# Kernel optimization log

Hardware: AMD Instinct MI355X
Metric: run time of the kernel (lower is better)

The kernel has to match this reference:

```python
import jax, jax.numpy as jnp
import numpy as np

N = 170000      # nodes (ogbn-arxiv scale)
E = 2720000     # edges (avg degree 16)
IN, H, L, OUT = 128, 256, 4, 40
BN_EPS = 1e-5


def setup_inputs() -> dict:
    key = jax.random.key(0)
    ks = jax.random.split(key, 6)
    x = jax.random.normal(ks[0], (N, IN), jnp.float32)
    edge_index = jax.random.randint(ks[1], (2, E), 0, N, dtype=jnp.int64)
    W_in = jax.random.normal(ks[2], (IN, H), jnp.float32) * 0.05
    b_in = jnp.zeros((H,), jnp.float32)
    W_hid = jax.random.normal(ks[3], (L - 1, H, H), jnp.float32) * 0.05
    b_hid = jnp.zeros((L - 1, H), jnp.float32)
    gamma = jnp.ones((L, H), jnp.float32)
    beta = jnp.zeros((L, H), jnp.float32)
    W_out = jax.random.normal(ks[4], (L * H, OUT), jnp.float32) * 0.05
    b_out = jnp.zeros((OUT,), jnp.float32)
    return dict(x=x, edge_index=edge_index, W_in=W_in, b_in=b_in,
                W_hid=W_hid, b_hid=b_hid, gamma=gamma, beta=beta,
                W_out=W_out, b_out=b_out)


def _gcn_aggregate(h, src, dst, norm_e, inv_deg):
    # message passing with symmetric normalization + self-loop term
    msg = h[src] * norm_e[:, None]                      # [E, H] gather
    agg = jax.ops.segment_sum(msg, dst, num_segments=N)  # [N, H] scatter-add
    return agg + h * inv_deg[:, None]                   # self-loop: deg^-1


def reference(x, edge_index, W_in, b_in, W_hid, b_hid, gamma, beta, W_out, b_out):
    src, dst = edge_index[0], edge_index[1]
    # degree (incl. self-loop), PyG gcn_norm style
    deg = jax.ops.segment_sum(jnp.ones((E,), x.dtype), dst, num_segments=N) + 1.0
    dinv = jax.lax.rsqrt(deg)
    norm_e = dinv[src] * dinv[dst]
    inv_deg = 1.0 / deg

    outs = []
    h = x
    for i in range(L):
        W = W_in if i == 0 else W_hid[i - 1]
        b = b_in if i == 0 else b_hid[i - 1]
        h = _gcn_aggregate(h @ W, src, dst, norm_e, inv_deg) + b
        # BatchNorm1d (training-mode batch statistics, biased variance)
        mean = jnp.mean(h, axis=0)
        var = jnp.mean(jnp.square(h - mean), axis=0)
        h = (h - mean) * jax.lax.rsqrt(var + BN_EPS) * gamma[i] + beta[i]
        h = jax.nn.relu(h)  # dropout is identity in eval mode
        outs.append(h)

    z = jnp.concatenate(outs, axis=-1) @ W_out + b_out  # JK 'cat' -> [N, L*H] @ [L*H, OUT]
    return jax.nn.log_softmax(z, axis=-1)
```

## Files before the change

kernel.cpp:

```cpp
#include <hip/hip_runtime.h>
#include <math.h>

constexpr int kN = 170000;
constexpr int kE = 2720000;
constexpr int kFin = 128;
constexpr int kFh = 256;
constexpr int kL = 4;
constexpr int kFout = 40;

typedef __attribute__((ext_vector_type(8))) short bf16x8;
typedef __attribute__((ext_vector_type(4))) float f32x4;

__device__ __forceinline__ float jk_b2f(unsigned short u) {
    unsigned int x = ((unsigned int)u) << 16;
    float f;
    __builtin_memcpy(&f, &x, 4);
    return f;
}
__device__ __forceinline__ unsigned short jk_f2b(float f) {
    unsigned int x;
    __builtin_memcpy(&x, &f, 4);
    unsigned int r = (x + 0x7fffu + ((x >> 16) & 1u)) >> 16;
    return (unsigned short)r;
}

union U4 {
    uint4 v;
    unsigned short s[8];
};

__global__ void jk5_zero_i(int* p, int n) {
    int i = blockIdx.x * blockDim.x + threadIdx.x;
    if (i < n) p[i] = 0;
}
__global__ void jk5_zero_f(float* p, int n) {
    int i = blockIdx.x * blockDim.x + threadIdx.x;
    if (i < n) p[i] = 0.0f;
}

__global__ void jk5_detect(const int* eb, int* flag) {
    __shared__ int nz;
    if (threadIdx.x == 0) nz = 0;
    __syncthreads();
    int bad = 0;
    for (int j = 0; j < 4; j++) {
        int idx = threadIdx.x * 4 + j;
        if (eb[2 * idx + 1] != 0) bad = 1;
    }
    if (bad) atomicOr(&nz, 1);
    __syncthreads();
    if (threadIdx.x == 0) {
        flag[0] = nz ? 0 : 1;
        flag[1] = 0;
    }
}

__global__ void jk5_count(const int* eb, const int* flag, int* counts, int* rank) {
    int e = blockIdx.x * blockDim.x + threadIdx.x;
    if (e >= kE) return;
    int s64 = flag[0];
    int d = eb[(kE + e) << s64];
    rank[e] = atomicAdd(&counts[d], 1);
}

__global__ void jk5_nodeprep(const int* counts, float* dinv, float* invdeg, int* off,
                             int* cursor) {
    int n = blockIdx.x * blockDim.x + threadIdx.x;
    if (n < kN) {
        int c = counts[n];
        float deg = (float)c + 1.0f;
        dinv[n] = rsqrtf(deg);
        invdeg[n] = 1.0f / deg;
        off[n] = atomicAdd(cursor, c);
    }
}

__global__ void jk5_fill(const int* eb, const int* flag, const int* rank, const int* off,
                         const float* dinv, int* csr_src, float* csr_w) {
    int e = blockIdx.x * blockDim.x + threadIdx.x;
    if (e >= kE) return;
    int s64 = flag[0];
    int s = eb[e << s64];
    int d = eb[(kE + e) << s64];
    int p = off[d] + rank[e];
    csr_src[p] = s;
    csr_w[p] = dinv[s] * dinv[d];
}

__global__ void jk5_wt(const float* W, unsigned short* Wt, int K) {
    int idx = blockIdx.x * blockDim.x + threadIdx.x;
    if (idx >= K * kFh) return;
    int c = idx / K, k = idx % K;
    Wt[idx] = jk_f2b(W[(size_t)k * kFh + c]);
}

__global__ void jk5_wtout(const float* Wout, unsigned short* Wto) {
    int idx = blockIdx.x * blockDim.x + threadIdx.x;
    if (idx >= kL * 48 * 256) return;
    int l = idx / (48 * 256);
    int rem = idx % (48 * 256);
    int col = rem >> 8, k = rem & 255;
    float wv = (col < kFout) ? Wout[(size_t)(l * kFh + k) * kFout + col] : 0.f;
    unsigned short hi = jk_f2b(wv);
    float res = wv - jk_b2f(hi);
    unsigned short lo = jk_f2b(res);
    Wto[((size_t)(l * 2 + 0) * 48 + col) * 256 + k] = hi;
    Wto[((size_t)(l * 2 + 1) * 48 + col) * 256 + k] = lo;
}

template <int AF32>
__global__ __launch_bounds__(256) void jk5_gemm(const void* Aptr, const unsigned short* Wt,
                                                unsigned short* C, int K) {
    __shared__ unsigned short As[128][40];
    __shared__ unsigned short Bs[128][40];
    int tid = threadIdx.x;
    int row0 = blockIdx.x * 128;
    int n0 = blockIdx.y * 128;
    int lane = tid & 63, w = tid >> 6;
    int wm = w >> 1, wn = w & 1;
    int lr = lane & 15, lg = lane >> 4;

    f32x4 acc[4][4];
#pragma unroll
    for (int i = 0; i < 4; i++)
#pragma unroll
        for (int j = 0; j < 4; j++) acc[i][j] = (f32x4){0.f, 0.f, 0.f, 0.f};

    int sr = tid >> 1;
    int skh = (tid & 1) * 16;

    for (int k0 = 0; k0 < K; k0 += 32) {
        {
            int row = row0 + sr;
            if (AF32) {
                const float* A = (const float*)Aptr;
                unsigned short tmp[16];
                if (row < kN) {
                    const float* g = A + (size_t)row * K + k0 + skh;
#pragma unroll
                    for (int j = 0; j < 16; j++) tmp[j] = jk_f2b(g[j]);
                } else {
#pragma unroll
                    for (int j = 0; j < 16; j++) tmp[j] = 0;
                }
                *(uint4*)&As[sr][skh] = *(uint4*)&tmp[0];
                *(uint4*)&As[sr][skh + 8] = *(uint4*)&tmp[8];
            } else {
                const unsigned short* A = (const unsigned short*)Aptr;
                uint4 u0 = make_uint4(0, 0, 0, 0), u1 = make_uint4(0, 0, 0, 0);
                if (row < kN) {
                    const unsigned short* g = A + (size_t)row * K + k0 + skh;
                    u0 = *(const uint4*)g;
                    u1 = *(const uint4*)(g + 8);
                }
                *(uint4*)&As[sr][skh] = u0;
                *(uint4*)&As[sr][skh + 8] = u1;
            }
        }
        {
            const unsigned short* g = Wt + (size_t)(n0 + sr) * K + k0 + skh;
            *(uint4*)&Bs[sr][skh] = *(const uint4*)g;
            *(uint4*)&Bs[sr][skh + 8] = *(const uint4*)(g + 8);
        }
        __syncthreads();

        bf16x8 af[4], bfr[4];
#pragma unroll
        for (int mi = 0; mi < 4; mi++)
            af[mi] = *(const bf16x8*)&As[wm * 64 + mi * 16 + lr][lg * 8];
#pragma unroll
        for (int ni = 0; ni < 4; ni++)
            bfr[ni] = *(const bf16x8*)&Bs[wn * 64 + ni * 16 + lr][lg * 8];
#pragma unroll
        for (int mi = 0; mi < 4; mi++)
#pragma unroll
            for (int ni = 0; ni < 4; ni++)
                acc[mi][ni] = __builtin_amdgcn_mfma_f32_16x16x32_bf16(af[mi], bfr[ni],
                                                                      acc[mi][ni], 0, 0, 0);
        __syncthreads();
    }

#pragma unroll
    for (int mi = 0; mi < 4; mi++) {
#pragma unroll
        for (int j = 0; j < 4; j++) {
            int row = row0 + wm * 64 + mi * 16 + lg * 4 + j;
            if (row < kN) {
#pragma unroll
                for (int ni = 0; ni < 4; ni++) {
                    int col = n0 + wn * 64 + ni * 16 + lr;
                    C[(size_t)row * kFh + col] = jk_f2b(acc[mi][ni][j]);
                }
            }
        }
    }
}

__global__ __launch_bounds__(256) void jk5_agg(const unsigned short* t, const float* bias,
                                               const int* off, const int* cnt, const int* csr_src,
                                               const float* csr_w, const float* invdeg,
                                               unsigned short* h, float* stats) {
    __shared__ float lsum[256], lsq[256];
    int tid = threadIdx.x;
    lsum[tid] = 0.f;
    lsq[tid] = 0.f;
    int lane32 = tid & 31;
    int grp = tid >> 5;
    int c0 = lane32 * 8;
    float bs[8];
#pragma unroll
    for (int j = 0; j < 8; j++) bs[j] = bias[c0 + j];

    float rsum[8] = {}, rsq[8] = {};

    for (int n = blockIdx.x * 8 + grp; n < kN; n += gridDim.x * 8) {
        float acc[8];
        {
            U4 u;
            u.v = *(const uint4*)(t + (size_t)n * kFh + c0);
            float sw = invdeg[n];
#pragma unroll
            for (int j = 0; j < 8; j++) acc[j] = sw * jk_b2f(u.s[j]);
        }
        int base = off[n], c = cnt[n];
        for (int i = 0; i < c; i += 4) {
            float w[4];
            U4 uu[4];
#pragma unroll
            for (int q = 0; q < 4; q++) {
                int e = i + q;
                bool v = e < c;
                int idx = v ? base + e : base;
                int src = csr_src[idx];
                w[q] = v ? csr_w[idx] : 0.0f;
                uu[q].v = *(const uint4*)(t + (size_t)src * kFh + c0);
            }
#pragma unroll
            for (int q = 0; q < 4; q++)
#pragma unroll
                for (int j = 0; j < 8; j++) acc[j] += w[q] * jk_b2f(uu[q].s[j]);
        }
        U4 o;
#pragma unroll
        for (int j = 0; j < 8; j++) {
            float v = acc[j] + bs[j];
            rsum[j] += v;
            rsq[j] += v * v;
            o.s[j] = jk_f2b(v);
        }
        *(uint4*)(h + (size_t)n * kFh + c0) = o.v;
    }

    __syncthreads();
#pragma unroll
    for (int j = 0; j < 8; j++) {
        atomicAdd(&lsum[c0 + j], rsum[j]);
        atomicAdd(&lsq[c0 + j], rsq[j]);
    }
    __syncthreads();
    atomicAdd(&stats[tid], lsum[tid]);
    atomicAdd(&stats[256 + tid], lsq[tid]);
}

__global__ void jk5_bnfinal(const float* stats, const float* gamma, const float* beta, int layer,
                            float* scale, float* shift) {
    int c = threadIdx.x;
    float mean = stats[c] / (float)kN;
    float var = stats[256 + c] / (float)kN - mean * mean;
    var = var < 0.f ? 0.f : var;
    float sc = gamma[layer * kFh + c] * rsqrtf(var + 1e-5f);
    scale[c] = sc;
    shift[c] = beta[layer * kFh + c] - mean * sc;
}

template <int FIRST, int LAST>
__global__ __launch_bounds__(256) void jk5_zacc(unsigned short* h, const float* scale,
                                                const float* shift, const unsigned short* Wto,
                                                const float* bout, float* z, float* out) {
    __shared__ unsigned short Bs[2][48][264];
    __shared__ unsigned short As[128][40];
    __shared__ float ssc[256], ssh[256];
    int tid = threadIdx.x;
    for (int f = tid; f < 2 * 48 * 256; f += 256) {
        int hl = f / (48 * 256);
        int rem = f % (48 * 256);
        Bs[hl][rem >> 8][rem & 255] = Wto[f];
    }
    ssc[tid] = scale[tid];
    ssh[tid] = shift[tid];
    __syncthreads();

    int row0 = blockIdx.x * 128;
    int w = tid >> 6, lane = tid & 63;
    int lr = lane & 15, lg = lane >> 4;
    int sr = tid >> 1, skh = (tid & 1) * 16;

    f32x4 acc[2][3];
#pragma unroll
    for (int mi = 0; mi < 2; mi++)
#pragma unroll
        for (int ni = 0; ni < 3; ni++) acc[mi][ni] = (f32x4){0.f, 0.f, 0.f, 0.f};

    for (int k0 = 0; k0 < kFh; k0 += 32) {
        int row = row0 + sr;
        U4 o0, o1;
        if (row < kN) {
            U4 u0, u1;
            const unsigned short* g = h + (size_t)row * kFh + k0 + skh;
            u0.v = *(const uint4*)g;
            u1.v = *(const uint4*)(g + 8);
#pragma unroll
            for (int j = 0; j < 8; j++) {
                float v = jk_b2f(u0.s[j]) * ssc[k0 + skh + j] + ssh[k0 + skh + j];
                o0.s[j] = jk_f2b(v > 0.f ? v : 0.f);
            }
#pragma unroll
            for (int j = 0; j < 8; j++) {
                float v = jk_b2f(u1.s[j]) * ssc[k0 + skh + 8 + j] + ssh[k0 + skh + 8 + j];
                o1.s[j] = jk_f2b(v > 0.f ? v : 0.f);
            }
            if (!LAST) {
                *(uint4*)(h + (size_t)row * kFh + k0 + skh) = o0.v;
                *(uint4*)(h + (size_t)row * kFh + k0 + skh + 8) = o1.v;
            }
        } else {
#pragma unroll
            for (int j = 0; j < 8; j++) { o0.s[j] = 0; o1.s[j] = 0; }
        }
        *(uint4*)&As[sr][skh] = o0.v;
        *(uint4*)&As[sr][skh + 8] = o1.v;
        __syncthreads();

        bf16x8 af[2], bh[3], bl[3];
#pragma unroll
        for (int mi = 0; mi < 2; mi++)
            af[mi] = *(const bf16x8*)&As[w * 32 + mi * 16 + lr][lg * 8];
#pragma unroll
        for (int ni = 0; ni < 3; ni++) {
            bh[ni] = *(const bf16x8*)&Bs[0][ni * 16 + lr][k0 + lg * 8];
            bl[ni] = *(const bf16x8*)&Bs[1][ni * 16 + lr][k0 + lg * 8];
        }
#pragma unroll
        for (int mi = 0; mi < 2; mi++)
#pragma unroll
            for (int ni = 0; ni < 3; ni++) {
                acc[mi][ni] = __builtin_amdgcn_mfma_f32_16x16x32_bf16(af[mi], bh[ni],
                                                                      acc[mi][ni], 0, 0, 0);
                acc[mi][ni] = __builtin_amdgcn_mfma_f32_16x16x32_bf16(af[mi], bl[ni],
                                                                      acc[mi][ni], 0, 0, 0);
            }
        __syncthreads();
    }

#pragma unroll
    for (int mi = 0; mi < 2; mi++) {
#pragma unroll
        for (int j = 0; j < 4; j++) {
            int row = row0 + w * 32 + mi * 16 + lg * 4 + j;
            if (row >= kN) continue;
            if (!LAST) {
#pragma unroll
                for (int ni = 0; ni < 3; ni++) {
                    int col = ni * 16 + lr;
                    if (col < kFout) {
                        if (FIRST)
                            z[(size_t)row * kFout + col] = acc[mi][ni][j] + bout[col];
                        else
                            z[(size_t)row * kFout + col] += acc[mi][ni][j];
                    }
                }
            } else {
                const float* zp = z + (size_t)row * kFout;
                float v0 = zp[lr] + acc[mi][0][j];
                float v1 = zp[16 + lr] + acc[mi][1][j];
                float v2 = (lr < 8) ? (zp[32 + lr] + acc[mi][2][j]) : -1e30f;
                float m = fmaxf(fmaxf(v0, v1), v2);
                m = fmaxf(m, __shfl_xor(m, 1, 64));
                m = fmaxf(m, __shfl_xor(m, 2, 64));
                m = fmaxf(m, __shfl_xor(m, 4, 64));
                m = fmaxf(m, __shfl_xor(m, 8, 64));
                float s = expf(v0 - m) + expf(v1 - m) + ((lr < 8) ? expf(v2 - m) : 0.f);
                s += __shfl_xor(s, 1, 64);
                s += __shfl_xor(s, 2, 64);
                s += __shfl_xor(s, 4, 64);
                s += __shfl_xor(s, 8, 64);
                float ls = m + logf(s);
                float* op = out + (size_t)row * kFout;
                op[lr] = v0 - ls;
                op[16 + lr] = v1 - ls;
                if (lr < 8) op[32 + lr] = v2 - ls;
            }
        }
    }
}

extern "C" void kernel_launch(void* const* d_in, const int* in_sizes, int n_in,
                              void* d_out, int out_size, void* d_ws, size_t ws_size,
                              hipStream_t stream) {
    (void)in_sizes; (void)n_in; (void)out_size; (void)ws_size;
    const float* x = (const float*)d_in[0];
    const int* eb = (const int*)d_in[1];
    const float* W_in = (const float*)d_in[2];
    const float* b_in = (const float*)d_in[3];
    const float* W_hid = (const float*)d_in[4];
    const float* b_hid = (const float*)d_in[5];
    const float* gamma = (const float*)d_in[6];
    const float* beta = (const float*)d_in[7];
    const float* W_out = (const float*)d_in[8];
    const float* b_out = (const float*)d_in[9];
    float* out = (float*)d_out;

    char* p = (char*)d_ws;
    auto alloc = [&](size_t b) -> void* {
        void* r = (void*)p;
        p += (b + 255) & ~(size_t)255;
        return r;
    };
    int* flag = (int*)alloc(8);
    int* counts = (int*)alloc((size_t)kN * 4);
    int* off = (int*)alloc((size_t)kN * 4);
    float* dinv = (float*)alloc((size_t)kN * 4);
    float* invdeg = (float*)alloc((size_t)kN * 4);
    float* bnsums = (float*)alloc((size_t)kL * 512 * 4);
    float* bnss = (float*)alloc((size_t)kL * 512 * 4);
    int* rank = (int*)alloc((size_t)kE * 4);
    int* csr_src = (int*)alloc((size_t)kE * 4);
    float* csr_w = (float*)alloc((size_t)kE * 4);
    unsigned short* hA = (unsigned short*)alloc((size_t)kN * kFh * 2);
    unsigned short* hB = (unsigned short*)alloc((size_t)kN * kFh * 2);
    float* z = (float*)alloc((size_t)kN * kFout * 4);
    unsigned short* Wt0 = (unsigned short*)alloc((size_t)kFin * kFh * 2);
    unsigned short* Wt1 = (unsigned short*)alloc((size_t)kFh * kFh * 2);
    unsigned short* Wt2 = (unsigned short*)alloc((size_t)kFh * kFh * 2);
    unsigned short* Wt3 = (unsigned short*)alloc((size_t)kFh * kFh * 2);
    unsigned short* Wto = (unsigned short*)alloc((size_t)kL * 2 * 48 * 256 * 2);

    jk5_zero_i<<<(kN + 255) / 256, 256, 0, stream>>>(counts, kN);
    jk5_zero_f<<<(kL * 512 + 255) / 256, 256, 0, stream>>>(bnsums, kL * 512);
    jk5_detect<<<1, 256, 0, stream>>>(eb, flag);
    jk5_count<<<(kE + 255) / 256, 256, 0, stream>>>(eb, flag, counts, rank);
    jk5_nodeprep<<<(kN + 255) / 256, 256, 0, stream>>>(counts, dinv, invdeg, off, flag + 1);
    jk5_fill<<<(kE + 255) / 256, 256, 0, stream>>>(eb, flag, rank, off, dinv, csr_src, csr_w);

    jk5_wt<<<(kFin * kFh + 255) / 256, 256, 0, stream>>>(W_in, Wt0, kFin);
    jk5_wt<<<(kFh * kFh + 255) / 256, 256, 0, stream>>>(W_hid, Wt1, kFh);
    jk5_wt<<<(kFh * kFh + 255) / 256, 256, 0, stream>>>(W_hid + (size_t)kFh * kFh, Wt2, kFh);
    jk5_wt<<<(kFh * kFh + 255) / 256, 256, 0, stream>>>(W_hid + (size_t)2 * kFh * kFh, Wt3, kFh);
    jk5_wtout<<<(kL * 48 * 256 + 255) / 256, 256, 0, stream>>>(W_out, Wto);

    unsigned short* Wts[4] = {Wt0, Wt1, Wt2, Wt3};
    dim3 gg((kN + 127) / 128, 2);
    int zg = (kN + 127) / 128;
    for (int l = 0; l < kL; l++) {
        const float* b = (l == 0) ? b_in : b_hid + (size_t)(l - 1) * kFh;
        int K = (l == 0) ? kFin : kFh;
        if (l == 0)
            jk5_gemm<1><<<gg, 256, 0, stream>>>(x, Wts[l], hA, K);
        else
            jk5_gemm<0><<<gg, 256, 0, stream>>>(hB, Wts[l], hA, K);
        jk5_agg<<<2560, 256, 0, stream>>>(hA, b, off, counts, csr_src, csr_w, invdeg, hB,
                                          bnsums + (size_t)l * 512);
        jk5_bnfinal<<<1, 256, 0, stream>>>(bnsums + (size_t)l * 512, gamma, beta, l,
                                           bnss + (size_t)l * 512, bnss + (size_t)l * 512 + 256);
        const unsigned short* wtl = Wto + (size_t)l * 2 * 48 * 256;
        float* sc = bnss + (size_t)l * 512;
        if (l == 0)
            jk5_zacc<1, 0><<<zg, 256, 0, stream>>>(hB, sc, sc + 256, wtl, b_out, z, out);
        else if (l < kL - 1)
            jk5_zacc<0, 0><<<zg, 256, 0, stream>>>(hB, sc, sc + 256, wtl, b_out, z, out);
        else
            jk5_zacc<0, 1><<<zg, 256, 0, stream>>>(hB, sc, sc + 256, wtl, b_out, z, out);
    }
}
```

Before: 1.924 ms.

## Split aggregation into one-node-per-wave kernel and separate BN stats pass

The aggregation kernel now gives each node one 64-lane wave. The two halves of the wave each process four edges per iteration and combine their partial sums with a cross-lane shuffle. The grid-stride loop with eight 32-lane groups per block is replaced by one block per four nodes. BatchNorm sum and sum-of-squares accumulation moves into a separate kernel that rereads the bf16 output. This is meant to expose more memory-level parallelism in the gather. In exchange it adds an extra full read of h per layer, and the statistics are now computed from bf16-rounded values.

```diff
diff --git a/kernel.cpp b/kernel.cpp
--- a/kernel.cpp
+++ b/kernel.cpp
@@ -29,16 +29,16 @@
     unsigned short s[8];
 };
 
-__global__ void jk5_zero_i(int* p, int n) {
+__global__ void jk6_zero_i(int* p, int n) {
     int i = blockIdx.x * blockDim.x + threadIdx.x;
     if (i < n) p[i] = 0;
 }
-__global__ void jk5_zero_f(float* p, int n) {
+__global__ void jk6_zero_f(float* p, int n) {
     int i = blockIdx.x * blockDim.x + threadIdx.x;
     if (i < n) p[i] = 0.0f;
 }
 
-__global__ void jk5_detect(const int* eb, int* flag) {
+__global__ void jk6_detect(const int* eb, int* flag) {
     __shared__ int nz;
     if (threadIdx.x == 0) nz = 0;
     __syncthreads();
@@ -55,7 +55,7 @@
     }
 }
 
-__global__ void jk5_count(const int* eb, const int* flag, int* counts, int* rank) {
+__global__ void jk6_count(const int* eb, const int* flag, int* counts, int* rank) {
     int e = blockIdx.x * blockDim.x + threadIdx.x;
     if (e >= kE) return;
     int s64 = flag[0];
@@ -63,7 +63,7 @@
     rank[e] = atomicAdd(&counts[d], 1);
 }
 
-__global__ void jk5_nodeprep(const int* counts, float* dinv, float* invdeg, int* off,
+__global__ void jk6_nodeprep(const int* counts, float* dinv, float* invdeg, int* off,
                              int* cursor) {
     int n = blockIdx.x * blockDim.x + threadIdx.x;
     if (n < kN) {
@@ -75,7 +75,7 @@
     }
 }
 
-__global__ void jk5_fill(const int* eb, const int* flag, const int* rank, const int* off,
+__global__ void jk6_fill(const int* eb, const int* flag, const int* rank, const int* off,
                          const float* dinv, int* csr_src, float* csr_w) {
     int e = blockIdx.x * blockDim.x + threadIdx.x;
     if (e >= kE) return;
@@ -87,14 +87,14 @@
     csr_w[p] = dinv[s] * dinv[d];
 }
 
-__global__ void jk5_wt(const float* W, unsigned short* Wt, int K) {
+__global__ void jk6_wt(const float* W, unsigned short* Wt, int K) {
     int idx = blockIdx.x * blockDim.x + threadIdx.x;
     if (idx >= K * kFh) return;
     int c = idx / K, k = idx % K;
     Wt[idx] = jk_f2b(W[(size_t)k * kFh + c]);
 }
 
-__global__ void jk5_wtout(const float* Wout, unsigned short* Wto) {
+__global__ void jk6_wtout(const float* Wout, unsigned short* Wto) {
     int idx = blockIdx.x * blockDim.x + threadIdx.x;
     if (idx >= kL * 48 * 256) return;
     int l = idx / (48 * 256);
@@ -109,7 +109,7 @@
 }
 
 template <int AF32>
-__global__ __launch_bounds__(256) void jk5_gemm(const void* Aptr, const unsigned short* Wt,
+__global__ __launch_bounds__(256) void jk6_gemm(const void* Aptr, const unsigned short* Wt,
                                                 unsigned short* C, int K) {
     __shared__ unsigned short As[128][40];
     __shared__ unsigned short Bs[128][40];
@@ -196,73 +196,86 @@
     }
 }
 
-__global__ __launch_bounds__(256) void jk5_agg(const unsigned short* t, const float* bias,
+__global__ __launch_bounds__(256) void jk6_agg(const unsigned short* t, const float* bias,
                                                const int* off, const int* cnt, const int* csr_src,
                                                const float* csr_w, const float* invdeg,
-                                               unsigned short* h, float* stats) {
+                                               unsigned short* h) {
+    int n = blockIdx.x * 4 + (threadIdx.x >> 6);
+    if (n >= kN) return;
+    int l = threadIdx.x & 63;
+    int half = l >> 5;
+    int c0 = (l & 31) * 8;
+
+    float acc[8];
+    {
+        U4 u;
+        u.v = *(const uint4*)(t + (size_t)n * kFh + c0);
+        float sw = half ? 0.0f : invdeg[n];
+#pragma unroll
+        for (int j = 0; j < 8; j++) acc[j] = sw * jk_b2f(u.s[j]);
+    }
+
+    int base = off[n], c = cnt[n];
+    for (int i = 0; i < c; i += 8) {
+        int e0 = i + half * 4;
+        float w[4];
+        U4 uu[4];
+#pragma unroll
+        for (int q = 0; q < 4; q++) {
+            int e = e0 + q;
+            bool v = e < c;
+            int idx = v ? base + e : base;
+            int src = csr_src[idx];
+            w[q] = v ? csr_w[idx] : 0.0f;
+            uu[q].v = *(const uint4*)(t + (size_t)src * kFh + c0);
+        }
+#pragma unroll
+        for (int q = 0; q < 4; q++)
+#pragma unroll
+            for (int j = 0; j < 8; j++) acc[j] += w[q] * jk_b2f(uu[q].s[j]);
+    }
+
+#pragma unroll
+    for (int j = 0; j < 8; j++) acc[j] += __shfl_xor(acc[j], 32, 64);
+
+    if (half == 0) {
+        U4 o;
+#pragma unroll
+        for (int j = 0; j < 8; j++) o.s[j] = jk_f2b(acc[j] + bias[c0 + j]);
+        *(uint4*)(h + (size_t)n * kFh + c0) = o.v;
+    }
+}
+
+__global__ __launch_bounds__(256) void jk6_bnstats(const unsigned short* h, float* stats) {
     __shared__ float lsum[256], lsq[256];
     int tid = threadIdx.x;
     lsum[tid] = 0.f;
     lsq[tid] = 0.f;
-    int lane32 = tid & 31;
+    __syncthreads();
+    int c0 = (tid & 31) * 8;
     int grp = tid >> 5;
-    int c0 = lane32 * 8;
-    float bs[8];
-#pragma unroll
-    for (int j = 0; j < 8; j++) bs[j] = bias[c0 + j];
-
-    float rsum[8] = {}, rsq[8] = {};
-
+    float rs[8] = {}, rq[8] = {};
     for (int n = blockIdx.x * 8 + grp; n < kN; n += gridDim.x * 8) {
-        float acc[8];
-        {
-            U4 u;
-            u.v = *(const uint4*)(t + (size_t)n * kFh + c0);
-            float sw = invdeg[n];
-#pragma unroll
-            for (int j = 0; j < 8; j++) acc[j] = sw * jk_b2f(u.s[j]);
-        }
-        int base = off[n], c = cnt[n];
-        for (int i = 0; i < c; i += 4) {
-            float w[4];
-            U4 uu[4];
-#pragma unroll
-            for (int q = 0; q < 4; q++) {
-                int e = i + q;
-                bool v = e < c;
-                int idx = v ? base + e : base;
-                int src = csr_src[idx];
-                w[q] = v ? csr_w[idx] : 0.0f;
-                uu[q].v = *(const uint4*)(t + (size_t)src * kFh + c0);
-            }
-#pragma unroll
-            for (int q = 0; q < 4; q++)
-#pragma unroll
-                for (int j = 0; j < 8; j++) acc[j] += w[q] * jk_b2f(uu[q].s[j]);
-        }
-        U4 o;
+        U4 u;
+        u.v = *(const uint4*)(h + (size_t)n * kFh + c0);
 #pragma unroll
         for (int j = 0; j < 8; j++) {
-            float v = acc[j] + bs[j];
-            rsum[j] += v;
-            rsq[j] += v * v;
-            o.s[j] = jk_f2b(v);
-        }
-        *(uint4*)(h + (size_t)n * kFh + c0) = o.v;
-    }
-
-    __syncthreads();
+            float v = jk_b2f(u.s[j]);
+            rs[j] += v;
+            rq[j] += v * v;
+        }
+    }
 #pragma unroll
     for (int j = 0; j < 8; j++) {
-        atomicAdd(&lsum[c0 + j], rsum[j]);
-        atomicAdd(&lsq[c0 + j], rsq[j]);
+        atomicAdd(&lsum[c0 + j], rs[j]);
+        atomicAdd(&lsq[c0 + j], rq[j]);
     }
     __syncthreads();
     atomicAdd(&stats[tid], lsum[tid]);
     atomicAdd(&stats[256 + tid], lsq[tid]);
 }
 
-__global__ void jk5_bnfinal(const float* stats, const float* gamma, const float* beta, int layer,
+__global__ void jk6_bnfinal(const float* stats, const float* gamma, const float* beta, int layer,
                             float* scale, float* shift) {
     int c = threadIdx.x;
     float mean = stats[c] / (float)kN;
@@ -274,7 +287,7 @@
 }
 
 template <int FIRST, int LAST>
-__global__ __launch_bounds__(256) void jk5_zacc(unsigned short* h, const float* scale,
+__global__ __launch_bounds__(256) void jk6_zacc(unsigned short* h, const float* scale,
                                                 const float* shift, const unsigned short* Wto,
                                                 const float* bout, float* z, float* out) {
     __shared__ unsigned short Bs[2][48][264];
@@ -435,18 +448,18 @@
     unsigned short* Wt3 = (unsigned short*)alloc((size_t)kFh * kFh * 2);
     unsigned short* Wto = (unsigned short*)alloc((size_t)kL * 2 * 48 * 256 * 2);
 
-    jk5_zero_i<<<(kN + 255) / 256, 256, 0, stream>>>(counts, kN);
-    jk5_zero_f<<<(kL * 512 + 255) / 256, 256, 0, stream>>>(bnsums, kL * 512);
-    jk5_detect<<<1, 256, 0, stream>>>(eb, flag);
-    jk5_count<<<(kE + 255) / 256, 256, 0, stream>>>(eb, flag, counts, rank);
-    jk5_nodeprep<<<(kN + 255) / 256, 256, 0, stream>>>(counts, dinv, invdeg, off, flag + 1);
-    jk5_fill<<<(kE + 255) / 256, 256, 0, stream>>>(eb, flag, rank, off, dinv, csr_src, csr_w);
-
-    jk5_wt<<<(kFin * kFh + 255) / 256, 256, 0, stream>>>(W_in, Wt0, kFin);
-    jk5_wt<<<(kFh * kFh + 255) / 256, 256, 0, stream>>>(W_hid, Wt1, kFh);
-    jk5_wt<<<(kFh * kFh + 255) / 256, 256, 0, stream>>>(W_hid + (size_t)kFh * kFh, Wt2, kFh);
-    jk5_wt<<<(kFh * kFh + 255) / 256, 256, 0, stream>>>(W_hid + (size_t)2 * kFh * kFh, Wt3, kFh);
-    jk5_wtout<<<(kL * 48 * 256 + 255) / 256, 256, 0, stream>>>(W_out, Wto);
+    jk6_zero_i<<<(kN + 255) / 256, 256, 0, stream>>>(counts, kN);
+    jk6_zero_f<<<(kL * 512 + 255) / 256, 256, 0, stream>>>(bnsums, kL * 512);
+    jk6_detect<<<1, 256, 0, stream>>>(eb, flag);
+    jk6_count<<<(kE + 255) / 256, 256, 0, stream>>>(eb, flag, counts, rank);
+    jk6_nodeprep<<<(kN + 255) / 256, 256, 0, stream>>>(counts, dinv, invdeg, off, flag + 1);
+    jk6_fill<<<(kE + 255) / 256, 256, 0, stream>>>(eb, flag, rank, off, dinv, csr_src, csr_w);
+
+    jk6_wt<<<(kFin * kFh + 255) / 256, 256, 0, stream>>>(W_in, Wt0, kFin);
+    jk6_wt<<<(kFh * kFh + 255) / 256, 256, 0, stream>>>(W_hid, Wt1, kFh);
+    jk6_wt<<<(kFh * kFh + 255) / 256, 256, 0, stream>>>(W_hid + (size_t)kFh * kFh, Wt2, kFh);
+    jk6_wt<<<(kFh * kFh + 255) / 256, 256, 0, stream>>>(W_hid + (size_t)2 * kFh * kFh, Wt3, kFh);
+    jk6_wtout<<<(kL * 48 * 256 + 255) / 256, 256, 0, stream>>>(W_out, Wto);
 
     unsigned short* Wts[4] = {Wt0, Wt1, Wt2, Wt3};
     dim3 gg((kN + 127) / 128, 2);
@@ -455,20 +468,20 @@
         const float* b = (l == 0) ? b_in : b_hid + (size_t)(l - 1) * kFh;
         int K = (l == 0) ? kFin : kFh;
         if (l == 0)
-            jk5_gemm<1><<<gg, 256, 0, stream>>>(x, Wts[l], hA, K);
+            jk6_gemm<1><<<gg, 256, 0, stream>>>(x, Wts[l], hA, K);
         else
-            jk5_gemm<0><<<gg, 256, 0, stream>>>(hB, Wts[l], hA, K);
-        jk5_agg<<<2560, 256, 0, stream>>>(hA, b, off, counts, csr_src, csr_w, invdeg, hB,
-                                          bnsums + (size_t)l * 512);
-        jk5_bnfinal<<<1, 256, 0, stream>>>(bnsums + (size_t)l * 512, gamma, beta, l,
+            jk6_gemm<0><<<gg, 256, 0, stream>>>(hB, Wts[l], hA, K);
+        jk6_agg<<<(kN + 3) / 4, 256, 0, stream>>>(hA, b, off, counts, csr_src, csr_w, invdeg, hB);
+        jk6_bnstats<<<1024, 256, 0, stream>>>(hB, bnsums + (size_t)l * 512);
+        jk6_bnfinal<<<1, 256, 0, stream>>>(bnsums + (size_t)l * 512, gamma, beta, l,
                                            bnss + (size_t)l * 512, bnss + (size_t)l * 512 + 256);
         const unsigned short* wtl = Wto + (size_t)l * 2 * 48 * 256;
         float* sc = bnss + (size_t)l * 512;
         if (l == 0)
-            jk5_zacc<1, 0><<<zg, 256, 0, stream>>>(hB, sc, sc + 256, wtl, b_out, z, out);
+            jk6_zacc<1, 0><<<zg, 256, 0, stream>>>(hB, sc, sc + 256, wtl, b_out, z, out);
         else if (l < kL - 1)
-            jk5_zacc<0, 0><<<zg, 256, 0, stream>>>(hB, sc, sc + 256, wtl, b_out, z, out);
+            jk6_zacc<0, 0><<<zg, 256, 0, stream>>>(hB, sc, sc + 256, wtl, b_out, z, out);
         else
-            jk5_zacc<0, 1><<<zg, 256, 0, stream>>>(hB, sc, sc + 256, wtl, b_out, z, out);
-    }
-}
+            jk6_zacc<0, 1><<<zg, 256, 0, stream>>>(hB, sc, sc + 256, wtl, b_out, z, out);
+    }
+}
```

Result: faster. 1.802 ms (-6.3%).
